# Kernel tuning notes

Measured on AMD Instinct MI355X. Metric: run time of the kernel, lower is better.

## Reference

```python
import jax, jax.numpy as jnp
import numpy as np

DIM = 1024
EPS = 1e-5

def layer_norm(x, gamma, beta):
    mu = jnp.mean(x, axis=-1, keepdims=True)
    var = jnp.mean(jnp.square(x - mu), axis=-1, keepdims=True)
    return (x - mu) * jax.lax.rsqrt(var + EPS) * gamma + beta

def setup_inputs() -> dict:
    key = jax.random.key(0)
    k1, k2 = jax.random.split(key)
    B, Nv, Nt = 8, 4096, 4096
    visual_tokens = jax.random.normal(k1, (B, Nv, DIM), dtype=jnp.float32)
    text_tokens = jax.random.normal(k2, (B, Nt, DIM), dtype=jnp.float32)
    gamma_v = jnp.ones((DIM,), dtype=jnp.float32)
    beta_v = jnp.zeros((DIM,), dtype=jnp.float32)
    gamma_t = jnp.ones((DIM,), dtype=jnp.float32)
    beta_t = jnp.zeros((DIM,), dtype=jnp.float32)
    return {"visual_tokens": visual_tokens, "text_tokens": text_tokens,
            "gamma_v": gamma_v, "beta_v": beta_v,
            "gamma_t": gamma_t, "beta_t": beta_t}

def reference(visual_tokens, text_tokens, gamma_v, beta_v, gamma_t, beta_t):
    # Dual LayerNorm
    V = layer_norm(visual_tokens, gamma_v, beta_v)   # [B, Nv, D]
    T = layer_norm(text_tokens, gamma_t, beta_t)     # [B, Nt, D]
    scale = jnp.sqrt(jnp.asarray(DIM, dtype=V.dtype))  # note: sqrt(dim), per source
    scores = jnp.einsum('bvd,btd->bvt', V, T) / scale  # [B, Nv, Nt]
    attn = jax.nn.softmax(scores, axis=-1)
    out = jnp.einsum('bvt,btd->bvd', attn, T)          # [B, Nv, D]
    return out
```

## Files before the change

### kernel.cpp

```cpp
#include <hip/hip_runtime.h>
#include <hip/hip_bf16.h>
#include <stdint.h>

#define DIMD 1024
#define NSEQ 4096
#define BATCH 8
#define LN_EPS 1e-5f

typedef __attribute__((ext_vector_type(8))) short bf16x8;
typedef __attribute__((ext_vector_type(4))) float f32x4;

__device__ __forceinline__ ushort f2bf(float f) {
  union { __hip_bfloat16 h; ushort u; } cv;
  cv.h = __float2bfloat16(f);
  return cv.u;
}

__device__ __forceinline__ void gload16(const void* g, void* l) {
  __builtin_amdgcn_global_load_lds(
      (const __attribute__((address_space(1))) uint32_t*)g,
      (__attribute__((address_space(3))) uint32_t*)l, 16, 0, 0);
}

#define MIDBAR()   asm volatile("s_barrier" ::: "memory")
#define ENDBAR()   asm volatile("s_waitcnt lgkmcnt(0)\n\ts_barrier" ::: "memory")
#define ENDBARV4() asm volatile("s_waitcnt vmcnt(4) lgkmcnt(0)\n\ts_barrier" ::: "memory")
#define ENDBARV0() asm volatile("s_waitcnt vmcnt(0) lgkmcnt(0)\n\ts_barrier" ::: "memory")

__device__ __forceinline__ int swz64(int byte) {
  return byte ^ (((byte >> 7) & 3) << 4);
}

__global__ __launch_bounds__(256) void ln_bf16_kernel(
    const float* __restrict__ x, const float* __restrict__ gamma,
    const float* __restrict__ beta, ushort* __restrict__ y, float scale)
{
  const int lane = threadIdx.x & 63;
  const int wv   = threadIdx.x >> 6;
  const size_t row = (size_t)blockIdx.x * 4 + wv;
  const float* xr = x + row * DIMD;

  float4 v[4];
#pragma unroll
  for (int c = 0; c < 4; ++c)
    v[c] = *(const float4*)(xr + c * 256 + lane * 4);

  float s = 0.f;
#pragma unroll
  for (int c = 0; c < 4; ++c) s += v[c].x + v[c].y + v[c].z + v[c].w;
#pragma unroll
  for (int m = 32; m >= 1; m >>= 1) s += __shfl_xor(s, m, 64);
  const float mean = s * (1.0f / DIMD);

  float vs = 0.f;
#pragma unroll
  for (int c = 0; c < 4; ++c) {
    float a0 = v[c].x - mean, a1 = v[c].y - mean;
    float a2 = v[c].z - mean, a3 = v[c].w - mean;
    vs += a0 * a0 + a1 * a1 + a2 * a2 + a3 * a3;
  }
#pragma unroll
  for (int m = 32; m >= 1; m >>= 1) vs += __shfl_xor(vs, m, 64);
  const float rstd = rsqrtf(vs * (1.0f / DIMD) + LN_EPS);

  ushort* yr = y + row * DIMD;
#pragma unroll
  for (int c = 0; c < 4; ++c) {
    const int d = c * 256 + lane * 4;
    float4 g  = *(const float4*)(gamma + d);
    float4 bb = *(const float4*)(beta + d);
    ushort4 o;
    o.x = f2bf(((v[c].x - mean) * rstd * g.x + bb.x) * scale);
    o.y = f2bf(((v[c].y - mean) * rstd * g.y + bb.y) * scale);
    o.z = f2bf(((v[c].z - mean) * rstd * g.z + bb.z) * scale);
    o.w = f2bf(((v[c].w - mean) * rstd * g.w + bb.w) * scale);
    *(ushort4*)(yr + d) = o;
  }
}

__global__ __launch_bounds__(256) void transpose_kernel(
    const ushort* __restrict__ src, ushort* __restrict__ dst)
{
  __shared__ ushort tile[64][72];
  const int t   = threadIdx.x;
  const int bid = blockIdx.x;
  const int b   = bid >> 10;
  const int rem = bid & 1023;
  const int n0  = (rem >> 4) << 6;
  const int d0  = (rem & 15) << 6;
  const ushort* sb = src + ((size_t)b * NSEQ) * DIMD;
  ushort* db       = dst + ((size_t)b * DIMD) * NSEQ;

#pragma unroll
  for (int k = 0; k < 2; ++k) {
    int c = t + 256 * k;
    int r = c >> 3, scol = (c & 7) * 8;
    *(uint4*)&tile[r][scol] =
        *(const uint4*)(sb + (size_t)(n0 + r) * DIMD + d0 + scol);
  }
  __syncthreads();
#pragma unroll
  for (int k = 0; k < 2; ++k) {
    int c = t + 256 * k;
    int dr = c >> 3, ns = (c & 7) * 8;
    union { ushort u[8]; uint4 q; } tv;
#pragma unroll
    for (int i = 0; i < 8; ++i) tv.u[i] = tile[ns + i][dr];
    *(uint4*)(db + (size_t)(d0 + dr) * NSEQ + n0 + ns) = tv.q;
  }
}

__device__ __forceinline__ void stage_chunk(const ushort* __restrict__ g,
                                            int ld, char* l, int tid) {
  const int o0 = tid * 16;
  const int o1 = o0 + 8192;
  const int s0 = swz64(o0);
  const int s1 = swz64(o1);
  gload16(g + (size_t)(s0 >> 6) * ld + ((s0 & 63) >> 1), l + o0);
  gload16(g + (size_t)(s1 >> 6) * ld + ((s1 & 63) >> 1), l + o1);
}

__device__ __forceinline__ bf16x8 ldsw_read(const char* base, int row, int lg) {
  return *(const bf16x8*)(base + swz64(row * 64 + lg * 16));
}

__device__ __forceinline__ void read_af(const char* Ac, int wm, int mh,
                                        int l15, int lg, bf16x8 (&af)[4]) {
#pragma unroll
  for (int m = 0; m < 4; ++m)
    af[m] = ldsw_read(Ac, wm * 128 + (mh * 4 + m) * 16 + l15, lg);
}
__device__ __forceinline__ void read_bf(const char* Bc, int wn,
                                        int l15, int lg, bf16x8 (&bf)[4]) {
#pragma unroll
  for (int n = 0; n < 4; ++n)
    bf[n] = ldsw_read(Bc, wn * 64 + n * 16 + l15, lg);
}

#define MFMA16(BASE)                                                          \
  do {                                                                        \
    MIDBAR();                                                                 \
    __builtin_amdgcn_s_setprio(1);                                            \
    _Pragma("unroll")                                                         \
    for (int m = 0; m < 4; ++m)                                               \
      _Pragma("unroll")                                                       \
      for (int n = 0; n < 4; ++n)                                             \
        acc[(BASE) + m][n] = __builtin_amdgcn_mfma_f32_16x16x32_bf16(         \
            af[m], bf[n], acc[(BASE) + m][n], 0, 0, 0);                       \
    __builtin_amdgcn_s_setprio(0);                                            \
  } while (0)

__device__ __forceinline__ void gemm_core_A(
    const ushort* __restrict__ Ab, const ushort* __restrict__ Bb,
    int lda, int ldb, int NT, char* smem, f32x4 (&acc)[8][4],
    int tid, int wm, int wn, int l15, int lg)
{
  stage_chunk(Ab,      lda, smem + 0,     tid);
  stage_chunk(Bb,      ldb, smem + 32768, tid);
  stage_chunk(Ab + 32, lda, smem + 16384, tid);
  stage_chunk(Bb + 32, ldb, smem + 49152, tid);
  ENDBARV4();

  for (int kt = 0; kt < NT; ++kt) {
    char* cb = smem + (kt & 1) * 65536;
    char* nbuf = smem + (((kt & 1) ^ 1) * 65536);
    const ushort* An = Ab + (size_t)(kt + 1) * 64;
    const ushort* Bn = Bb + (size_t)(kt + 1) * 64;
    const bool pf = (kt + 1 < NT);
    bf16x8 af[4], bf[4];

    read_af(cb + 0, wm, 0, l15, lg, af);
    read_bf(cb + 32768, wn, l15, lg, bf);
    if (pf) stage_chunk(An, lda, nbuf + 0, tid);
    MFMA16(0);
    ENDBAR();

    read_af(cb + 0, wm, 1, l15, lg, af);
    if (pf) stage_chunk(Bn, ldb, nbuf + 32768, tid);
    MFMA16(4);
    if (pf) { ENDBARV4(); } else { ENDBARV0(); }

    read_af(cb + 16384, wm, 0, l15, lg, af);
    read_bf(cb + 49152, wn, l15, lg, bf);
    if (pf) stage_chunk(An + 32, lda, nbuf + 16384, tid);
    MFMA16(0);
    ENDBAR();

    read_af(cb + 16384, wm, 1, l15, lg, af);
    if (pf) stage_chunk(Bn + 32, ldb, nbuf + 49152, tid);
    MFMA16(4);
    if (pf) { ENDBARV4(); } else { ENDBAR(); }
  }
}

__device__ __forceinline__ void gemm_core_B(
    const ushort* __restrict__ Ab, const ushort* __restrict__ Bb,
    int lda, int ldb, int NT, char* smem, f32x4 (&acc)[8][4],
    int tid, int wm, int wn, int l15, int lg)
{
  char* buf0 = smem;
  char* buf1 = smem + 65536;

  stage_chunk(Ab,      lda, buf0 + 0,     tid);
  stage_chunk(Bb,      ldb, buf0 + 32768, tid);
  stage_chunk(Ab + 32, lda, buf0 + 16384, tid);
  stage_chunk(Bb + 32, ldb, buf0 + 49152, tid);
  stage_chunk(Ab + 64, lda, buf1 + 0,     tid);
  stage_chunk(Bb + 64, ldb, buf1 + 32768, tid);
  asm volatile("s_waitcnt vmcnt(4)\n\ts_barrier" ::: "memory");

  for (int T = 0; T < NT; T += 2) {
    const bool pf = (T + 2 < NT);
    const ushort* A1s = Ab + (size_t)(T + 1) * 64;
    const ushort* B1s = Bb + (size_t)(T + 1) * 64;
    const ushort* A2s = Ab + (size_t)(T + 2) * 64;
    const ushort* B2s = Bb + (size_t)(T + 2) * 64;
    const ushort* A3s = Ab + (size_t)(T + 3) * 64;
    const ushort* B3s = Bb + (size_t)(T + 3) * 64;
    bf16x8 af[4], bf[4];

    read_af(buf0 + 0, wm, 0, l15, lg, af);
    read_bf(buf0 + 32768, wn, l15, lg, bf);
    stage_chunk(A1s + 32, lda, buf1 + 16384, tid);
    MFMA16(0);
    ENDBAR();

    read_af(buf0 + 0, wm, 1, l15, lg, af);
    stage_chunk(B1s + 32, ldb, buf1 + 49152, tid);
    MFMA16(4);
    ENDBAR();

    read_af(buf0 + 16384, wm, 0, l15, lg, af);
    read_bf(buf0 + 49152, wn, l15, lg, bf);
    if (pf) stage_chunk(A2s, lda, buf0 + 0, tid);
    MFMA16(0);
    ENDBAR();

    read_af(buf0 + 16384, wm, 1, l15, lg, af);
    if (pf) stage_chunk(B2s, ldb, buf0 + 32768, tid);
    MFMA16(4);
    if (pf) { ENDBARV4(); } else { ENDBARV0(); }

    read_af(buf1 + 0, wm, 0, l15, lg, af);
    read_bf(buf1 + 32768, wn, l15, lg, bf);
    if (pf) stage_chunk(A2s + 32, lda, buf0 + 16384, tid);
    MFMA16(0);
    ENDBAR();

    read_af(buf1 + 0, wm, 1, l15, lg, af);
    if (pf) stage_chunk(B2s + 32, ldb, buf0 + 49152, tid);
    MFMA16(4);
    ENDBAR();

    read_af(buf1 + 16384, wm, 0, l15, lg, af);
    read_bf(buf1 + 49152, wn, l15, lg, bf);
    if (pf) stage_chunk(A3s, lda, buf1 + 0, tid);
    MFMA16(0);
    ENDBAR();

    read_af(buf1 + 16384, wm, 1, l15, lg, af);
    if (pf) stage_chunk(B3s, ldb, buf1 + 32768, tid);
    MFMA16(4);
    if (pf) { ENDBARV4(); } else { ENDBARV0(); }
  }
}

__global__ __launch_bounds__(512, 2) void gemm1_256(
    const ushort* __restrict__ Q, const ushort* __restrict__ K,
    ushort* __restrict__ S, float* __restrict__ Rsum,
    int b0, size_t s_stride)
{
  extern __shared__ char smem[];
  const int tid  = threadIdx.x;
  const int lane = tid & 63;
  const int wave = tid >> 6;
  const int wm = wave >> 2, wn = wave & 3;
  const int l15 = lane & 15, lg = lane >> 4;

  int bx, by, bzc;
  if (gridDim.z == BATCH) {
    const int hw = blockIdx.x + (blockIdx.y << 4) + (blockIdx.z << 8);
    bzc = hw & 7;
    const int inner = hw >> 3;
    bx = inner & 15; by = (inner >> 4) & 15;
  } else {
    bx = blockIdx.x; by = blockIdx.y; bzc = 0;
  }

  const int bz   = b0 + bzc;
  const int row0 = by * 256, col0 = bx * 256;
  const ushort* Qb = Q + (size_t)bz * NSEQ * DIMD + (size_t)row0 * DIMD;
  const ushort* Kb = K + (size_t)bz * NSEQ * DIMD + (size_t)col0 * DIMD;

  f32x4 acc[8][4];
#pragma unroll
  for (int m = 0; m < 8; ++m)
#pragma unroll
    for (int n = 0; n < 4; ++n) acc[m][n] = 0.0f;

  gemm_core_B(Kb, Qb, DIMD, DIMD, DIMD / 64, smem, acc, tid, wm, wn, l15, lg);

  ushort* Sb = S + (size_t)bzc * s_stride;
  float*  Rs = Rsum + (size_t)bz * NSEQ;
  float vsum[4] = {0.f, 0.f, 0.f, 0.f};
#pragma unroll
  for (int ti = 0; ti < 8; ++ti) {
#pragma unroll
    for (int vi = 0; vi < 4; ++vi) {
      const int v = row0 + wn * 64 + vi * 16 + l15;
      const int t = col0 + wm * 128 + ti * 16 + lg * 4;
      float p0 = __expf(acc[ti][vi][0]);
      float p1 = __expf(acc[ti][vi][1]);
      float p2 = __expf(acc[ti][vi][2]);
      float p3 = __expf(acc[ti][vi][3]);
      vsum[vi] += (p0 + p1) + (p2 + p3);
      unsigned long long pk =
          (unsigned long long)f2bf(p0)        |
          ((unsigned long long)f2bf(p1) << 16) |
          ((unsigned long long)f2bf(p2) << 32) |
          ((unsigned long long)f2bf(p3) << 48);
      *(unsigned long long*)(Sb + (size_t)v * NSEQ + t) = pk;
    }
  }
#pragma unroll
  for (int vi = 0; vi < 4; ++vi) {
    float s = vsum[vi];
    s += __shfl_xor(s, 16, 64);
    s += __shfl_xor(s, 32, 64);
    if (lg == 0)
      atomicAdd(Rs + row0 + wn * 64 + vi * 16 + l15, s);
  }
}

__global__ __launch_bounds__(512, 2) void gemm2_256(
    const ushort* __restrict__ S, const ushort* __restrict__ Kt,
    const float* __restrict__ Rsum, float* __restrict__ Out,
    int b0, size_t s_stride)
{
  extern __shared__ char smem[];
  const int tid  = threadIdx.x;
  const int lane = tid & 63;
  const int wave = tid >> 6;
  const int wm = wave >> 2, wn = wave & 3;
  const int l15 = lane & 15, lg = lane >> 4;

  int bx, by, bzc;
  if (gridDim.z == BATCH) {
    const int hw = blockIdx.x + (blockIdx.y << 2) + (blockIdx.z << 6);
    bzc = hw & 7;
    const int inner = hw >> 3;
    bx = inner & 3; by = inner >> 2;
  } else {
    bx = blockIdx.x; by = blockIdx.y; bzc = 0;
  }

  const int bz   = b0 + bzc;
  const int row0 = by * 256;
  const int col0 = bx * 256;
  const ushort* Sb2 = S  + (size_t)bzc * s_stride + (size_t)row0 * NSEQ;
  const ushort* Vtb = Kt + ((size_t)bz * DIMD + col0) * NSEQ;

  f32x4 acc[8][4];
#pragma unroll
  for (int m = 0; m < 8; ++m)
#pragma unroll
    for (int n = 0; n < 4; ++n) acc[m][n] = 0.0f;

  gemm_core_A(Vtb, Sb2, NSEQ, NSEQ, NSEQ / 64, smem, acc, tid, wm, wn, l15, lg);

  const float* Rs = Rsum + (size_t)bz * NSEQ;
  float* Ob = Out + (size_t)bz * NSEQ * DIMD;
  float inv[4];
#pragma unroll
  for (int vi = 0; vi < 4; ++vi)
    inv[vi] = 1.0f / Rs[row0 + wn * 64 + vi * 16 + l15];
#pragma unroll
  for (int di = 0; di < 8; ++di) {
#pragma unroll
    for (int vi = 0; vi < 4; ++vi) {
      const int v = row0 + wn * 64 + vi * 16 + l15;
      const int d = col0 + wm * 128 + di * 16 + lg * 4;
      f32x4 o = acc[di][vi] * inv[vi];
      __builtin_nontemporal_store(
          o, (f32x4*)(Ob + (size_t)v * DIMD + d));
    }
  }
}

extern "C" void kernel_launch(void* const* d_in, const int* in_sizes, int n_in,
                              void* d_out, int out_size, void* d_ws, size_t ws_size,
                              hipStream_t stream) {
  const float* vis = (const float*)d_in[0];
  const float* txt = (const float*)d_in[1];
  const float* gv  = (const float*)d_in[2];
  const float* bv  = (const float*)d_in[3];
  const float* gt  = (const float*)d_in[4];
  const float* bt  = (const float*)d_in[5];
  float* out = (float*)d_out;

  const size_t tokens = (size_t)BATCH * NSEQ * DIMD;
  ushort* Qbf = (ushort*)d_ws;
  ushort* Kbf = Qbf + tokens;
  ushort* Ktb = Kbf + tokens;
  char*   wsb = (char*)d_ws;
  float*  Rsum = (float*)(wsb + 201326592);
  ushort* Sbuf = (ushort*)(wsb + 201457664);

  const size_t S_FULL = (size_t)BATCH * NSEQ * NSEQ * 2;
  const size_t NEED_FULL = 201457664 + S_FULL;

  ln_bf16_kernel<<<BATCH * NSEQ / 4, 256, 0, stream>>>(vis, gv, bv, Qbf, 0.03125f);
  ln_bf16_kernel<<<BATCH * NSEQ / 4, 256, 0, stream>>>(txt, gt, bt, Kbf, 1.0f);
  transpose_kernel<<<BATCH * (NSEQ / 64) * (DIMD / 64), 256, 0, stream>>>(Kbf, Ktb);

  hipFuncSetAttribute((const void*)gemm1_256,
                      hipFuncAttributeMaxDynamicSharedMemorySize, 131072);
  hipFuncSetAttribute((const void*)gemm2_256,
                      hipFuncAttributeMaxDynamicSharedMemorySize, 131072);

  hipMemsetAsync(Rsum, 0, (size_t)BATCH * NSEQ * sizeof(float), stream);

  if (ws_size >= NEED_FULL) {
    gemm1_256<<<dim3(16, 16, BATCH), 512, 131072, stream>>>(
        Qbf, Kbf, Sbuf, Rsum, 0, (size_t)NSEQ * NSEQ);
    gemm2_256<<<dim3(4, 16, BATCH), 512, 131072, stream>>>(
        Sbuf, Ktb, Rsum, out, 0, (size_t)NSEQ * NSEQ);
  } else {
    for (int b = 0; b < BATCH; ++b) {
      gemm1_256<<<dim3(16, 16, 1), 512, 131072, stream>>>(
          Qbf, Kbf, Sbuf, Rsum, b, 0);
      gemm2_256<<<dim3(4, 16, 1), 512, 131072, stream>>>(
          Sbuf, Ktb, Rsum, out, b, 0);
    }
  }
}
```

Baseline: 674.4 us.

## Store score tiles pre-swizzled in LDS image layout for linear staging in second GEMM

```diff
diff --git a/kernel.cpp b/kernel.cpp
--- a/kernel.cpp
+++ b/kernel.cpp
@@ -9,11 +9,16 @@
 
 typedef __attribute__((ext_vector_type(8))) short bf16x8;
 typedef __attribute__((ext_vector_type(4))) float f32x4;
+typedef __attribute__((ext_vector_type(4))) unsigned int u32x4;
 
 __device__ __forceinline__ ushort f2bf(float f) {
   union { __hip_bfloat16 h; ushort u; } cv;
   cv.h = __float2bfloat16(f);
   return cv.u;
+}
+
+__device__ __forceinline__ float fexp2(float x) {
+  return exp2f(x);
 }
 
 __device__ __forceinline__ void gload16(const void* g, void* l) {
@@ -118,6 +123,12 @@
   const int s1 = swz64(o1);
   gload16(g + (size_t)(s0 >> 6) * ld + ((s0 & 63) >> 1), l + o0);
   gload16(g + (size_t)(s1 >> 6) * ld + ((s1 & 63) >> 1), l + o1);
+}
+
+__device__ __forceinline__ void stage_lin(const ushort* __restrict__ g,
+                                          char* l, int tid) {
+  gload16(g + tid * 8,        l + tid * 16);
+  gload16(g + 4096 + tid * 8, l + tid * 16 + 8192);
 }
 
 __device__ __forceinline__ bf16x8 ldsw_read(const char* base, int row, int lg) {
@@ -150,22 +161,26 @@
     __builtin_amdgcn_s_setprio(0);                                            \
   } while (0)
 
+template <bool LINB>
 __device__ __forceinline__ void gemm_core_A(
     const ushort* __restrict__ Ab, const ushort* __restrict__ Bb,
     int lda, int ldb, int NT, char* smem, f32x4 (&acc)[8][4],
     int tid, int wm, int wn, int l15, int lg)
 {
-  stage_chunk(Ab,      lda, smem + 0,     tid);
-  stage_chunk(Bb,      ldb, smem + 32768, tid);
+  stage_chunk(Ab, lda, smem + 0, tid);
+  if (LINB) stage_lin(Bb, smem + 32768, tid);
+  else      stage_chunk(Bb, ldb, smem + 32768, tid);
   stage_chunk(Ab + 32, lda, smem + 16384, tid);
-  stage_chunk(Bb + 32, ldb, smem + 49152, tid);
+  if (LINB) stage_lin(Bb + 8192, smem + 49152, tid);
+  else      stage_chunk(Bb + 32, ldb, smem + 49152, tid);
   ENDBARV4();
 
   for (int kt = 0; kt < NT; ++kt) {
     char* cb = smem + (kt & 1) * 65536;
     char* nbuf = smem + (((kt & 1) ^ 1) * 65536);
     const ushort* An = Ab + (size_t)(kt + 1) * 64;
-    const ushort* Bn = Bb + (size_t)(kt + 1) * 64;
+    const ushort* Bn = LINB ? (Bb + (size_t)(kt + 1) * 16384)
+                            : (Bb + (size_t)(kt + 1) * 64);
     const bool pf = (kt + 1 < NT);
     bf16x8 af[4], bf[4];
 
@@ -176,7 +191,10 @@
     ENDBAR();
 
     read_af(cb + 0, wm, 1, l15, lg, af);
-    if (pf) stage_chunk(Bn, ldb, nbuf + 32768, tid);
+    if (pf) {
+      if (LINB) stage_lin(Bn, nbuf + 32768, tid);
+      else      stage_chunk(Bn, ldb, nbuf + 32768, tid);
+    }
     MFMA16(4);
     if (pf) { ENDBARV4(); } else { ENDBARV0(); }
 
@@ -187,81 +205,12 @@
     ENDBAR();
 
     read_af(cb + 16384, wm, 1, l15, lg, af);
-    if (pf) stage_chunk(Bn + 32, ldb, nbuf + 49152, tid);
+    if (pf) {
+      if (LINB) stage_lin(Bn + 8192, nbuf + 49152, tid);
+      else      stage_chunk(Bn + 32, ldb, nbuf + 49152, tid);
+    }
     MFMA16(4);
     if (pf) { ENDBARV4(); } else { ENDBAR(); }
-  }
-}
-
-__device__ __forceinline__ void gemm_core_B(
-    const ushort* __restrict__ Ab, const ushort* __restrict__ Bb,
-    int lda, int ldb, int NT, char* smem, f32x4 (&acc)[8][4],
-    int tid, int wm, int wn, int l15, int lg)
-{
-  char* buf0 = smem;
-  char* buf1 = smem + 65536;
-
-  stage_chunk(Ab,      lda, buf0 + 0,     tid);
-  stage_chunk(Bb,      ldb, buf0 + 32768, tid);
-  stage_chunk(Ab + 32, lda, buf0 + 16384, tid);
-  stage_chunk(Bb + 32, ldb, buf0 + 49152, tid);
-  stage_chunk(Ab + 64, lda, buf1 + 0,     tid);
-  stage_chunk(Bb + 64, ldb, buf1 + 32768, tid);
-  asm volatile("s_waitcnt vmcnt(4)\n\ts_barrier" ::: "memory");
-
-  for (int T = 0; T < NT; T += 2) {
-    const bool pf = (T + 2 < NT);
-    const ushort* A1s = Ab + (size_t)(T + 1) * 64;
-    const ushort* B1s = Bb + (size_t)(T + 1) * 64;
-    const ushort* A2s = Ab + (size_t)(T + 2) * 64;
-    const ushort* B2s = Bb + (size_t)(T + 2) * 64;
-    const ushort* A3s = Ab + (size_t)(T + 3) * 64;
-    const ushort* B3s = Bb + (size_t)(T + 3) * 64;
-    bf16x8 af[4], bf[4];
-
-    read_af(buf0 + 0, wm, 0, l15, lg, af);
-    read_bf(buf0 + 32768, wn, l15, lg, bf);
-    stage_chunk(A1s + 32, lda, buf1 + 16384, tid);
-    MFMA16(0);
-    ENDBAR();
-
-    read_af(buf0 + 0, wm, 1, l15, lg, af);
-    stage_chunk(B1s + 32, ldb, buf1 + 49152, tid);
-    MFMA16(4);
-    ENDBAR();
-
-    read_af(buf0 + 16384, wm, 0, l15, lg, af);
-    read_bf(buf0 + 49152, wn, l15, lg, bf);
-    if (pf) stage_chunk(A2s, lda, buf0 + 0, tid);
-    MFMA16(0);
-    ENDBAR();
-
-    read_af(buf0 + 16384, wm, 1, l15, lg, af);
-    if (pf) stage_chunk(B2s, ldb, buf0 + 32768, tid);
-    MFMA16(4);
-    if (pf) { ENDBARV4(); } else { ENDBARV0(); }
-
-    read_af(buf1 + 0, wm, 0, l15, lg, af);
-    read_bf(buf1 + 32768, wn, l15, lg, bf);
-    if (pf) stage_chunk(A2s + 32, lda, buf0 + 16384, tid);
-    MFMA16(0);
-    ENDBAR();
-
-    read_af(buf1 + 0, wm, 1, l15, lg, af);
-    if (pf) stage_chunk(B2s + 32, ldb, buf0 + 49152, tid);
-    MFMA16(4);
-    ENDBAR();
-
-    read_af(buf1 + 16384, wm, 0, l15, lg, af);
-    read_bf(buf1 + 49152, wn, l15, lg, bf);
-    if (pf) stage_chunk(A3s, lda, buf1 + 0, tid);
-    MFMA16(0);
-    ENDBAR();
-
-    read_af(buf1 + 16384, wm, 1, l15, lg, af);
-    if (pf) stage_chunk(B3s, ldb, buf1 + 32768, tid);
-    MFMA16(4);
-    if (pf) { ENDBARV4(); } else { ENDBARV0(); }
   }
 }
 
@@ -298,30 +247,44 @@
 #pragma unroll
     for (int n = 0; n < 4; ++n) acc[m][n] = 0.0f;
 
-  gemm_core_B(Kb, Qb, DIMD, DIMD, DIMD / 64, smem, acc, tid, wm, wn, l15, lg);
-
-  ushort* Sb = S + (size_t)bzc * s_stride;
-  float*  Rs = Rsum + (size_t)bz * NSEQ;
+  gemm_core_A<false>(Kb, Qb, DIMD, DIMD, DIMD / 64, smem, acc, tid, wm, wn, l15, lg);
+
   float vsum[4] = {0.f, 0.f, 0.f, 0.f};
 #pragma unroll
   for (int ti = 0; ti < 8; ++ti) {
+    const int tl   = wm * 128 + ti * 16 + lg * 4;
+    const int ktl  = tl >> 6;
+    const int half = (tl >> 5) & 1;
+    const int tcol = tl & 31;
+    char* img = smem + (ktl * 2 + half) * 16384;
 #pragma unroll
     for (int vi = 0; vi < 4; ++vi) {
-      const int v = row0 + wn * 64 + vi * 16 + l15;
-      const int t = col0 + wm * 128 + ti * 16 + lg * 4;
-      float p0 = __expf(acc[ti][vi][0]);
-      float p1 = __expf(acc[ti][vi][1]);
-      float p2 = __expf(acc[ti][vi][2]);
-      float p3 = __expf(acc[ti][vi][3]);
+      const int vrow = wn * 64 + vi * 16 + l15;
+      float p0 = fexp2(acc[ti][vi][0]);
+      float p1 = fexp2(acc[ti][vi][1]);
+      float p2 = fexp2(acc[ti][vi][2]);
+      float p3 = fexp2(acc[ti][vi][3]);
       vsum[vi] += (p0 + p1) + (p2 + p3);
       unsigned long long pk =
           (unsigned long long)f2bf(p0)        |
           ((unsigned long long)f2bf(p1) << 16) |
           ((unsigned long long)f2bf(p2) << 32) |
           ((unsigned long long)f2bf(p3) << 48);
-      *(unsigned long long*)(Sb + (size_t)v * NSEQ + t) = pk;
-    }
-  }
+      *(unsigned long long*)(img + swz64(vrow * 64 + tcol * 2)) = pk;
+    }
+  }
+  __syncthreads();
+
+  ushort* region = S + (size_t)bzc * s_stride
+                 + (size_t)by * 1048576 + (size_t)bx * 65536;
+#pragma unroll
+  for (int j = 0; j < 16; ++j) {
+    const int off = (j * 512 + tid) * 16;
+    u32x4 vle = *(const u32x4*)(smem + off);
+    __builtin_nontemporal_store(vle, (u32x4*)((char*)region + off));
+  }
+
+  float* Rs = Rsum + (size_t)bz * NSEQ;
 #pragma unroll
   for (int vi = 0; vi < 4; ++vi) {
     float s = vsum[vi];
@@ -357,7 +320,7 @@
   const int bz   = b0 + bzc;
   const int row0 = by * 256;
   const int col0 = bx * 256;
-  const ushort* Sb2 = S  + (size_t)bzc * s_stride + (size_t)row0 * NSEQ;
+  const ushort* Sbase = S + (size_t)bzc * s_stride + (size_t)by * 1048576;
   const ushort* Vtb = Kt + ((size_t)bz * DIMD + col0) * NSEQ;
 
   f32x4 acc[8][4];
@@ -366,7 +329,7 @@
 #pragma unroll
     for (int n = 0; n < 4; ++n) acc[m][n] = 0.0f;
 
-  gemm_core_A(Vtb, Sb2, NSEQ, NSEQ, NSEQ / 64, smem, acc, tid, wm, wn, l15, lg);
+  gemm_core_A<true>(Vtb, Sbase, NSEQ, 0, NSEQ / 64, smem, acc, tid, wm, wn, l15, lg);
 
   const float* Rs = Rsum + (size_t)bz * NSEQ;
   float* Ob = Out + (size_t)bz * NSEQ * DIMD;
@@ -381,8 +344,7 @@
       const int v = row0 + wn * 64 + vi * 16 + l15;
       const int d = col0 + wm * 128 + di * 16 + lg * 4;
       f32x4 o = acc[di][vi] * inv[vi];
-      __builtin_nontemporal_store(
-          o, (f32x4*)(Ob + (size_t)v * DIMD + d));
+      *(f32x4*)(Ob + (size_t)v * DIMD + d) = o;
     }
   }
 }
@@ -409,16 +371,17 @@
   const size_t S_FULL = (size_t)BATCH * NSEQ * NSEQ * 2;
   const size_t NEED_FULL = 201457664 + S_FULL;
 
-  ln_bf16_kernel<<<BATCH * NSEQ / 4, 256, 0, stream>>>(vis, gv, bv, Qbf, 0.03125f);
+  ln_bf16_kernel<<<BATCH * NSEQ / 4, 256, 0, stream>>>(vis, gv, bv, Qbf,
+                                                       0.045084219f);
   ln_bf16_kernel<<<BATCH * NSEQ / 4, 256, 0, stream>>>(txt, gt, bt, Kbf, 1.0f);
   transpose_kernel<<<BATCH * (NSEQ / 64) * (DIMD / 64), 256, 0, stream>>>(Kbf, Ktb);
 
-  hipFuncSetAttribute((const void*)gemm1_256,
+  (void)hipFuncSetAttribute((const void*)gemm1_256,
                       hipFuncAttributeMaxDynamicSharedMemorySize, 131072);
-  hipFuncSetAttribute((const void*)gemm2_256,
+  (void)hipFuncSetAttribute((const void*)gemm2_256,
                       hipFuncAttributeMaxDynamicSharedMemorySize, 131072);
 
-  hipMemsetAsync(Rsum, 0, (size_t)BATCH * NSEQ * sizeof(float), stream);
+  (void)hipMemsetAsync(Rsum, 0, (size_t)BATCH * NSEQ * sizeof(float), stream);
 
   if (ws_size >= NEED_FULL) {
     gemm1_256<<<dim3(16, 16, BATCH), 512, 131072, stream>>>(
```

New measurement: 634.6 us. -5.9%, faster.
